# Optimization experiments

Hardware: AMD Instinct MI355X
Metric: run time of the kernel (lower is better)

## Reference

```python
import jax, jax.numpy as jnp
import numpy as np

N = 50000   # nodes (subjects in population graph)
E = 800000  # edges (similarity graph, avg degree 16)
F = 128     # node features


def setup_inputs() -> dict:
    key = jax.random.key(0)
    ks = jax.random.split(key, 8)

    def glorot(k, shape):
        scale = 1.0 / np.sqrt(shape[0])
        return jax.random.normal(k, shape, jnp.float32) * scale

    x = jax.random.normal(ks[0], (N, F), jnp.float32)
    edge_index = jax.random.randint(ks[1], (2, E), 0, N, dtype=jnp.int64)
    return {
        "x": x,
        "edge_index": edge_index,
        "W1": glorot(ks[2], (F, 128)),   "b1": jnp.zeros((128,), jnp.float32),
        "W2": glorot(ks[3], (128, 64)),  "b2": jnp.zeros((64,), jnp.float32),
        "Wf1": glorot(ks[4], (64, 32)),  "bf1": jnp.zeros((32,), jnp.float32),
        "Wf2": glorot(ks[5], (32, 1)),   "bf2": jnp.zeros((1,), jnp.float32),
    }


def reference(x, edge_index, W1, b1, W2, b2, Wf1, bf1, Wf2, bf2):
    n = x.shape[0]
    # GCNConv (PyG default): add self-loops, symmetric deg^{-1/2} normalization
    loops = jnp.arange(n, dtype=edge_index.dtype)
    src = jnp.concatenate([edge_index[0], loops])  # [E+N]
    dst = jnp.concatenate([edge_index[1], loops])  # [E+N]
    deg = jax.ops.segment_sum(jnp.ones_like(dst, x.dtype), dst, num_segments=n)
    dinv = deg ** -0.5  # deg >= 1 thanks to self-loops
    norm = (dinv[src] * dinv[dst])[:, None]  # [E+N, 1]

    def gcn_conv(h, W, b):
        h = h @ W                                    # transform [n, out]
        msg = h[src] * norm                          # gather + normalize
        agg = jax.ops.segment_sum(msg, dst, num_segments=n)  # scatter-add
        return agg + b

    h = jnp.tanh(gcn_conv(x, W1, b1))
    h = jnp.tanh(gcn_conv(h, W2, b2))
    h = jnp.tanh(h @ Wf1 + bf1)
    return h @ Wf2 + bf2  # [n, 1] brain-age prediction
```

## Files before the change

kernel.cpp:

```cpp
#include <hip/hip_runtime.h>
#include <hip/hip_fp16.h>
#include <math.h>

#define TPB 256
#define CAP 64
#define BSHIFT 7
#define BSPAN 128
#define NBLK 512
#define BCAP 3072

typedef int   nt_i4 __attribute__((ext_vector_type(4)));
typedef unsigned nt_u4 __attribute__((ext_vector_type(4)));
typedef _Float16 f16x8 __attribute__((ext_vector_type(8)));
typedef float f32x4 __attribute__((ext_vector_type(4)));

__global__ __launch_bounds__(TPB) void init_pre(const int* __restrict__ e,
                                                int* __restrict__ flag,
                                                int* __restrict__ gcur, int nbuck) {
  __shared__ int found;
  if (threadIdx.x == 0) found = 0;
  __syncthreads();
  for (int b = threadIdx.x; b < nbuck; b += TPB) gcur[b] = 0;
  int nz = 0;
  for (int k = threadIdx.x; k < 2048; k += TPB)
    nz |= (e[2 * k + 1] != 0) ? 1 : 0;
  if (nz) atomicOr(&found, 1);
  __syncthreads();
  if (threadIdx.x == 0) *flag = found;
}

__device__ __forceinline__ void load_edge(const void* eptr, int flag, int E,
                                          int e, int& s, int& d) {
  if (flag) {
    const int* p = (const int*)eptr;
    s = p[e];
    d = p[E + e];
  } else {
    const long long* p = (const long long*)eptr;
    s = (int)p[e];
    d = (int)p[E + e];
  }
}

__device__ __forceinline__ void load_edge4(const void* eptr, int flag, int E,
                                           int e0, int* s, int* d) {
  if (flag) {
    const int* p = (const int*)eptr;
    nt_i4 sv = __builtin_nontemporal_load((const nt_i4*)&p[e0]);
    nt_i4 dv = __builtin_nontemporal_load((const nt_i4*)&p[E + e0]);
    s[0] = sv.x; s[1] = sv.y; s[2] = sv.z; s[3] = sv.w;
    d[0] = dv.x; d[1] = dv.y; d[2] = dv.z; d[3] = dv.w;
  } else {
    const long long* p = (const long long*)eptr;
    nt_i4 sa = __builtin_nontemporal_load((const nt_i4*)&p[e0]);
    nt_i4 sb = __builtin_nontemporal_load((const nt_i4*)&p[e0 + 2]);
    nt_i4 da = __builtin_nontemporal_load((const nt_i4*)&p[E + e0]);
    nt_i4 db = __builtin_nontemporal_load((const nt_i4*)&p[E + e0 + 2]);
    s[0] = sa.x; s[1] = sa.z; s[2] = sb.x; s[3] = sb.z;
    d[0] = da.x; d[1] = da.z; d[2] = db.x; d[3] = db.z;
  }
}

__global__ __launch_bounds__(TPB) void bucket_pairs(const void* __restrict__ eptr,
                                                    const int* __restrict__ flag,
                                                    int* __restrict__ gcur,
                                                    unsigned long long* __restrict__ pairs,
                                                    int E, int nbuck, int chunk) {
  extern __shared__ int lds[];
  int* hist = lds;
  int* cur = lds + nbuck;
  const int tid = threadIdx.x;
  const int fl = *flag;
  for (int b = tid; b < nbuck; b += TPB) hist[b] = 0;
  __syncthreads();

  const int start = blockIdx.x * chunk;
  const int end = min(E, start + chunk);

  for (int e0 = start + tid * 4; e0 < end; e0 += TPB * 4) {
    if (e0 + 4 <= end) {
      int s[4], d[4];
      load_edge4(eptr, fl, E, e0, s, d);
#pragma unroll
      for (int j = 0; j < 4; j++) atomicAdd(&hist[d[j] >> BSHIFT], 1);
    } else {
      for (int e = e0; e < end; e++) {
        int s, d;
        load_edge(eptr, fl, E, e, s, d);
        atomicAdd(&hist[d >> BSHIFT], 1);
      }
    }
  }
  __syncthreads();

  for (int b = tid; b < nbuck; b += TPB) {
    int c = hist[b];
    cur[b] = (c > 0) ? (b * BCAP + atomicAdd(&gcur[b], c)) : 0;
  }
  __syncthreads();

  for (int e0 = start + tid * 4; e0 < end; e0 += TPB * 4) {
    if (e0 + 4 <= end) {
      int s[4], d[4];
      load_edge4(eptr, fl, E, e0, s, d);
#pragma unroll
      for (int j = 0; j < 4; j++) {
        int slot = atomicAdd(&cur[d[j] >> BSHIFT], 1);
        unsigned long long pv =
            ((unsigned long long)(unsigned)d[j] << 32) | (unsigned)s[j];
        __builtin_nontemporal_store(pv, &pairs[slot]);
      }
    } else {
      for (int e = e0; e < end; e++) {
        int s, d;
        load_edge(eptr, fl, E, e, s, d);
        int slot = atomicAdd(&cur[d >> BSHIFT], 1);
        unsigned long long pv =
            ((unsigned long long)(unsigned)d << 32) | (unsigned)s;
        __builtin_nontemporal_store(pv, &pairs[slot]);
      }
    }
  }
}

__global__ __launch_bounds__(TPB) void ell_from_pairs(const unsigned long long* __restrict__ pairs,
                                                      const int* __restrict__ gcur,
                                                      int* __restrict__ ell,
                                                      int* __restrict__ degi, int n) {
  __shared__ int cnt[BSPAN];
  const int b = blockIdx.x;
  const int tid = threadIdx.x;
  const int base = b << BSHIFT;
  for (int j = tid; j < BSPAN; j += TPB) cnt[j] = 0;
  __syncthreads();
  const int npair = min(gcur[b], BCAP);
  const unsigned long long* pp = &pairs[(size_t)b * BCAP];
  for (int i = tid; i < npair; i += TPB) {
    unsigned long long pr = __builtin_nontemporal_load(&pp[i]);
    int d = (int)(pr >> 32);
    int s = (int)(unsigned)pr;
    int slot = atomicAdd(&cnt[d - base], 1);
    if (slot < CAP) ell[(size_t)d * CAP + slot] = s;
  }
  __syncthreads();
  for (int j = tid; j < BSPAN; j += TPB) {
    int node = base + j;
    if (node < n) degi[node] = cnt[j];
  }
}

template <int NC, typename AT>
__global__ __launch_bounds__(TPB, 4) void gemm_mfma(const AT* __restrict__ A,
                                                    const float* __restrict__ W,
                                                    const int* __restrict__ degi,
                                                    __half* __restrict__ out, int nrows) {
  constexpr int K = 128;
  constexpr int WT = 136;
  constexpr int NT = NC / 16;
  __shared__ _Float16 Wt[NC * WT];

  const int tid = threadIdx.x;

  for (int idx = tid; idx < NC * (K / 2); idx += TPB) {
    int c = idx % NC;
    int p = idx / NC;
    float w0 = W[(2 * p) * NC + c];
    float w1 = W[(2 * p + 1) * NC + c];
    __half2* dst = (__half2*)&Wt[c * WT + 2 * p];
    *dst = __floats2half2_rn(w0, w1);
  }
  __syncthreads();

  const int w = tid >> 6;
  const int lane = tid & 63;
  const int l15 = lane & 15;
  const int q = lane >> 4;
  const int m_base = blockIdx.x * 64 + w * 16;
  const int m = m_base + l15;
  const bool mok = m < nrows;

  f32x4 acc[NT];
#pragma unroll
  for (int t = 0; t < NT; t++) acc[t] = (f32x4){0.f, 0.f, 0.f, 0.f};

#pragma unroll
  for (int ks = 0; ks < 4; ks++) {
    const int k0 = ks * 32;
    f16x8 a;
    if (sizeof(AT) == 4) {
      float4 f0 = make_float4(0.f, 0.f, 0.f, 0.f), f1 = f0;
      if (mok) {
        const float* ap = (const float*)A + (size_t)m * K + k0 + q * 8;
        f0 = *(const float4*)ap;
        f1 = *(const float4*)(ap + 4);
      }
      a[0] = (_Float16)f0.x; a[1] = (_Float16)f0.y;
      a[2] = (_Float16)f0.z; a[3] = (_Float16)f0.w;
      a[4] = (_Float16)f1.x; a[5] = (_Float16)f1.y;
      a[6] = (_Float16)f1.z; a[7] = (_Float16)f1.w;
    } else {
      union { uint4 u; f16x8 h; } ld;
      ld.u = make_uint4(0, 0, 0, 0);
      if (mok)
        ld.u = *(const uint4*)((const __half*)A + (size_t)m * K + k0 + q * 8);
      a = ld.h;
    }
#pragma unroll
    for (int t = 0; t < NT; t++) {
      f16x8 b = *(const f16x8*)&Wt[(t * 16 + l15) * WT + k0 + q * 8];
      acc[t] = __builtin_amdgcn_mfma_f32_16x16x32_f16(a, b, acc[t], 0, 0, 0);
    }
  }

#pragma unroll
  for (int r = 0; r < 4; r++) {
    int row = m_base + q * 4 + r;
    if (row >= nrows) continue;
    float di = rsqrtf((float)(degi[row] + 1));
#pragma unroll
    for (int t = 0; t < NT; t++)
      out[(size_t)row * NC + t * 16 + l15] = (__half)(acc[t][r] * di);
  }
}

__global__ __launch_bounds__(TPB) void gcn_agg1_fused(const int* __restrict__ degi,
                                                      const int* __restrict__ ell,
                                                      const __half* __restrict__ t,
                                                      const float* __restrict__ bias,
                                                      const float* __restrict__ W2,
                                                      __half* __restrict__ t2, int n) {
  constexpr int NC = 128, LPN = 16, CPL = 8, NPB = TPB / LPN;
  constexpr int WT = 136;
  __shared__ _Float16 Wt2[64 * WT];
  __shared__ _Float16 Ah[NPB * WT];

  const int tid = threadIdx.x;

  for (int idx = tid; idx < 64 * 64; idx += TPB) {
    int c = idx & 63;
    int p = idx >> 6;
    float w0 = W2[(2 * p) * 64 + c];
    float w1 = W2[(2 * p + 1) * 64 + c];
    *(__half2*)&Wt2[c * WT + 2 * p] = __floats2half2_rn(w0, w1);
  }

  const int g = tid / LPN;
  const int ll = tid % LPN;
  const int node = blockIdx.x * NPB + g;
  const bool active = node < n;

  if (active) {
    int dg = degi[node];
    float di = rsqrtf((float)(dg + 1));
    int deg = dg > CAP ? CAP : dg;
    const int* nbr = &ell[(size_t)node * CAP];
    const __half* tp = t + (size_t)ll * CPL;

    float acc[CPL];
#pragma unroll
    for (int c = 0; c < CPL; c++) acc[c] = 0.f;

    union Ld { uint4 u4; __half2 h[4]; };
    auto addv = [&](const Ld& v) {
#pragma unroll
      for (int c = 0; c < 4; c++) {
        float2 f = __half22float2(v.h[c]);
        acc[2 * c] += f.x;
        acc[2 * c + 1] += f.y;
      }
    };

    int j = 0;
    for (; j + 8 <= deg; j += 8) {
      nt_i4 n0 = __builtin_nontemporal_load((const nt_i4*)&nbr[j]);
      nt_i4 n1 = __builtin_nontemporal_load((const nt_i4*)&nbr[j + 4]);
      Ld v0, v1, v2, v3, v4, v5, v6, v7;
      v0.u4 = *(const uint4*)&tp[(size_t)n0.x * NC];
      v1.u4 = *(const uint4*)&tp[(size_t)n0.y * NC];
      v2.u4 = *(const uint4*)&tp[(size_t)n0.z * NC];
      v3.u4 = *(const uint4*)&tp[(size_t)n0.w * NC];
      v4.u4 = *(const uint4*)&tp[(size_t)n1.x * NC];
      v5.u4 = *(const uint4*)&tp[(size_t)n1.y * NC];
      v6.u4 = *(const uint4*)&tp[(size_t)n1.z * NC];
      v7.u4 = *(const uint4*)&tp[(size_t)n1.w * NC];
      addv(v0); addv(v1); addv(v2); addv(v3);
      addv(v4); addv(v5); addv(v6); addv(v7);
    }
    for (; j + 4 <= deg; j += 4) {
      nt_i4 n0 = __builtin_nontemporal_load((const nt_i4*)&nbr[j]);
      Ld v0, v1, v2, v3;
      v0.u4 = *(const uint4*)&tp[(size_t)n0.x * NC];
      v1.u4 = *(const uint4*)&tp[(size_t)n0.y * NC];
      v2.u4 = *(const uint4*)&tp[(size_t)n0.z * NC];
      v3.u4 = *(const uint4*)&tp[(size_t)n0.w * NC];
      addv(v0); addv(v1); addv(v2); addv(v3);
    }
    for (; j < deg; j++) {
      Ld v;
      v.u4 = *(const uint4*)&tp[(size_t)nbr[j] * NC];
      addv(v);
    }
    {
      Ld v;
      v.u4 = *(const uint4*)&tp[(size_t)node * NC];
      addv(v);
    }

    const float* bp = &bias[ll * CPL];
    float bv[CPL];
#pragma unroll
    for (int c = 0; c < CPL; c += 4) {
      float4 b = *(const float4*)&bp[c];
      bv[c] = b.x; bv[c + 1] = b.y; bv[c + 2] = b.z; bv[c + 3] = b.w;
    }
    union { _Float16 h[8]; f16x8 v; } o;
#pragma unroll
    for (int c = 0; c < CPL; c++)
      o.h[c] = (_Float16)tanhf(acc[c] * di + bv[c]);
    *(f16x8*)&Ah[g * WT + ll * CPL] = o.v;
  }
  __syncthreads();

  const int w = tid >> 6;
  const int lane = tid & 63;
  const int l15 = lane & 15;
  const int q = lane >> 4;
  f32x4 acc2 = (f32x4){0.f, 0.f, 0.f, 0.f};
#pragma unroll
  for (int ks = 0; ks < 4; ks++) {
    f16x8 a = *(const f16x8*)&Ah[l15 * WT + ks * 32 + q * 8];
    f16x8 b = *(const f16x8*)&Wt2[(w * 16 + l15) * WT + ks * 32 + q * 8];
    acc2 = __builtin_amdgcn_mfma_f32_16x16x32_f16(a, b, acc2, 0, 0, 0);
  }
#pragma unroll
  for (int r = 0; r < 4; r++) {
    int rn = blockIdx.x * NPB + q * 4 + r;
    if (rn < n) {
      float d2 = rsqrtf((float)(degi[rn] + 1));
      t2[(size_t)rn * 64 + w * 16 + l15] = (__half)(acc2[r] * d2);
    }
  }
}

__global__ __launch_bounds__(TPB) void gcn_aggregate_head(
    const int* __restrict__ degi, const int* __restrict__ ell,
    const __half* __restrict__ t, const float* __restrict__ b2,
    const float* __restrict__ Wf1, const float* __restrict__ bf1,
    const float* __restrict__ Wf2, const float* __restrict__ bf2,
    float* __restrict__ out, int n) {
  constexpr int NC = 64, LPN = 16, NPB = TPB / LPN;
  __shared__ float hrow[NPB][68];
  __shared__ float Wf1s[64 * 32];
  __shared__ float Wf2s[32];
  const int tid = threadIdx.x;

#pragma unroll
  for (int i = 0; i < 2; i++) {
    int lid = tid + i * TPB;
    *(float4*)&Wf1s[lid * 4] = *(const float4*)&Wf1[lid * 4];
  }
  if (tid < 32) Wf2s[tid] = Wf2[tid];

  const int g = tid / LPN;
  const int ll = tid % LPN;
  const int node = blockIdx.x * NPB + g;
  const bool active = node < n;

  float acc[4] = {0.f, 0.f, 0.f, 0.f};
  if (active) {
    int dg = degi[node];
    float di = rsqrtf((float)(dg + 1));
    int deg = dg > CAP ? CAP : dg;
    const int* nbr = &ell[(size_t)node * CAP];
    const __half* tp = t + (size_t)ll * 4;
    union Ld { uint2 u2; __half2 h[2]; };
    auto addv = [&](const Ld& v) {
      float2 f0 = __half22float2(v.h[0]);
      float2 f1 = __half22float2(v.h[1]);
      acc[0] += f0.x; acc[1] += f0.y; acc[2] += f1.x; acc[3] += f1.y;
    };
    int j = 0;
    for (; j + 8 <= deg; j += 8) {
      nt_i4 n0 = __builtin_nontemporal_load((const nt_i4*)&nbr[j]);
      nt_i4 n1 = __builtin_nontemporal_load((const nt_i4*)&nbr[j + 4]);
      Ld v0, v1, v2, v3, v4, v5, v6, v7;
      v0.u2 = *(const uint2*)&tp[(size_t)n0.x * NC];
      v1.u2 = *(const uint2*)&tp[(size_t)n0.y * NC];
      v2.u2 = *(const uint2*)&tp[(size_t)n0.z * NC];
      v3.u2 = *(const uint2*)&tp[(size_t)n0.w * NC];
      v4.u2 = *(const uint2*)&tp[(size_t)n1.x * NC];
      v5.u2 = *(const uint2*)&tp[(size_t)n1.y * NC];
      v6.u2 = *(const uint2*)&tp[(size_t)n1.z * NC];
      v7.u2 = *(const uint2*)&tp[(size_t)n1.w * NC];
      addv(v0); addv(v1); addv(v2); addv(v3);
      addv(v4); addv(v5); addv(v6); addv(v7);
    }
    for (; j + 4 <= deg; j += 4) {
      nt_i4 nn = __builtin_nontemporal_load((const nt_i4*)&nbr[j]);
      Ld v0, v1, v2, v3;
      v0.u2 = *(const uint2*)&tp[(size_t)nn.x * NC];
      v1.u2 = *(const uint2*)&tp[(size_t)nn.y * NC];
      v2.u2 = *(const uint2*)&tp[(size_t)nn.z * NC];
      v3.u2 = *(const uint2*)&tp[(size_t)nn.w * NC];
      addv(v0); addv(v1); addv(v2); addv(v3);
    }
    for (; j < deg; j++) {
      Ld v;
      v.u2 = *(const uint2*)&tp[(size_t)nbr[j] * NC];
      addv(v);
    }
    {
      Ld v;
      v.u2 = *(const uint2*)&tp[(size_t)node * NC];
      addv(v);
    }
    float4 b = *(const float4*)&b2[ll * 4];
    hrow[g][ll * 4 + 0] = tanhf(acc[0] * di + b.x);
    hrow[g][ll * 4 + 1] = tanhf(acc[1] * di + b.y);
    hrow[g][ll * 4 + 2] = tanhf(acc[2] * di + b.z);
    hrow[g][ll * 4 + 3] = tanhf(acc[3] * di + b.w);
  }
  __syncthreads();

  float hid0 = bf1[ll];
  float hid1 = bf1[ll + 16];
#pragma unroll 8
  for (int i = 0; i < 64; i++) {
    float hv = hrow[g][i];
    hid0 += hv * Wf1s[i * 32 + ll];
    hid1 += hv * Wf1s[i * 32 + ll + 16];
  }
  float p = tanhf(hid0) * Wf2s[ll] + tanhf(hid1) * Wf2s[ll + 16];
  p += __shfl_down(p, 8, 16);
  p += __shfl_down(p, 4, 16);
  p += __shfl_down(p, 2, 16);
  p += __shfl_down(p, 1, 16);
  if (active && ll == 0) out[node] = p + bf2[0];
}

extern "C" void kernel_launch(void* const* d_in, const int* in_sizes, int n_in,
                              void* d_out, int out_size, void* d_ws, size_t ws_size,
                              hipStream_t stream) {
  const float* x   = (const float*)d_in[0];
  const void*  eix = d_in[1];
  const float* W1  = (const float*)d_in[2];
  const float* b1  = (const float*)d_in[3];
  const float* W2  = (const float*)d_in[4];
  const float* b2  = (const float*)d_in[5];
  const float* Wf1 = (const float*)d_in[6];
  const float* bf1 = (const float*)d_in[7];
  const float* Wf2 = (const float*)d_in[8];
  const float* bf2 = (const float*)d_in[9];
  float* out = (float*)d_out;

  const int N = in_sizes[0] / 128;
  const int E = in_sizes[1] / 2;
  const int nbuck = (N + BSPAN - 1) >> BSHIFT;
  int chunk = (E + NBLK - 1) / NBLK;
  chunk = (chunk + 3) & ~3;
  const size_t ldsBytes = (size_t)nbuck * 2 * 4;

  char* ws = (char*)d_ws;
  size_t off = 0;
  int* degi = (int*)(ws + off); off += (size_t)N * 4;
  int* flag = (int*)(ws + off); off += 64;
  int* gcur = (int*)(ws + off); off += (size_t)(nbuck + 16) * 4;
  off = (off + 15) & ~(size_t)15;
  unsigned long long* pairs = (unsigned long long*)(ws + off);
  off += (size_t)nbuck * BCAP * 8;
  int* ell = (int*)(ws + off); off += (size_t)N * CAP * 4;
  off = (off + 15) & ~(size_t)15;
  __half* t1 = (__half*)(ws + off); off += (size_t)N * 128 * 2;
  __half* t2 = (__half*)(ws + off); off += (size_t)N * 64 * 2;
  (void)ws_size; (void)n_in; (void)out_size;

  init_pre<<<1, TPB, 0, stream>>>((const int*)eix, flag, gcur, nbuck);
  bucket_pairs<<<NBLK, TPB, ldsBytes, stream>>>(eix, flag, gcur, pairs, E, nbuck, chunk);
  ell_from_pairs<<<nbuck, TPB, 0, stream>>>(pairs, gcur, ell, degi, N);

  gemm_mfma<128, float><<<(N + 63) / 64, TPB, 0, stream>>>(x, W1, degi, t1, N);

  gcn_agg1_fused<<<(N + 15) / 16, TPB, 0, stream>>>(degi, ell, t1, b1, W2, t2, N);

  gcn_aggregate_head<<<(N + 15) / 16, TPB, 0, stream>>>(degi, ell, t2, b2,
                                                        Wf1, bf1, Wf2, bf2, out, N);
}
```

Before: 227.7 us.

## Split layer-1 aggregation into two column-half passes and unfuse W2 GEMM

Replaces the fused layer-1 aggregate+W2 kernel with two launches that each gather a 64-column half of t1, so each pass has a smaller working set that fits the cache better. The tanh output goes to a new h1 buffer with nontemporal stores, and a separate gemm_mfma<64, __half> launch then applies W2. This removes the per-block W2 LDS staging and the block barrier. In exchange it adds extra launches, a 2-byte-per-element h1 write and reread, and reads every neighbor index list twice.

```diff
diff --git a/kernel.cpp b/kernel.cpp
--- a/kernel.cpp
+++ b/kernel.cpp
@@ -223,123 +223,88 @@
   }
 }
 
-__global__ __launch_bounds__(TPB) void gcn_agg1_fused(const int* __restrict__ degi,
-                                                      const int* __restrict__ ell,
-                                                      const __half* __restrict__ t,
-                                                      const float* __restrict__ bias,
-                                                      const float* __restrict__ W2,
-                                                      __half* __restrict__ t2, int n) {
-  constexpr int NC = 128, LPN = 16, CPL = 8, NPB = TPB / LPN;
-  constexpr int WT = 136;
-  __shared__ _Float16 Wt2[64 * WT];
-  __shared__ _Float16 Ah[NPB * WT];
-
+template <int HALF>
+__global__ __launch_bounds__(TPB) void gcn_agg1_half(const int* __restrict__ degi,
+                                                     const int* __restrict__ ell,
+                                                     const __half* __restrict__ t,
+                                                     const float* __restrict__ bias,
+                                                     __half* __restrict__ h1, int n) {
+  constexpr int NC = 128, LPN = 8, CPL = 8, NPB = TPB / LPN;
   const int tid = threadIdx.x;
-
-  for (int idx = tid; idx < 64 * 64; idx += TPB) {
-    int c = idx & 63;
-    int p = idx >> 6;
-    float w0 = W2[(2 * p) * 64 + c];
-    float w1 = W2[(2 * p + 1) * 64 + c];
-    *(__half2*)&Wt2[c * WT + 2 * p] = __floats2half2_rn(w0, w1);
-  }
-
   const int g = tid / LPN;
   const int ll = tid % LPN;
   const int node = blockIdx.x * NPB + g;
-  const bool active = node < n;
-
-  if (active) {
-    int dg = degi[node];
-    float di = rsqrtf((float)(dg + 1));
-    int deg = dg > CAP ? CAP : dg;
-    const int* nbr = &ell[(size_t)node * CAP];
-    const __half* tp = t + (size_t)ll * CPL;
-
-    float acc[CPL];
-#pragma unroll
-    for (int c = 0; c < CPL; c++) acc[c] = 0.f;
-
-    union Ld { uint4 u4; __half2 h[4]; };
-    auto addv = [&](const Ld& v) {
-#pragma unroll
-      for (int c = 0; c < 4; c++) {
-        float2 f = __half22float2(v.h[c]);
-        acc[2 * c] += f.x;
-        acc[2 * c + 1] += f.y;
-      }
-    };
-
-    int j = 0;
-    for (; j + 8 <= deg; j += 8) {
-      nt_i4 n0 = __builtin_nontemporal_load((const nt_i4*)&nbr[j]);
-      nt_i4 n1 = __builtin_nontemporal_load((const nt_i4*)&nbr[j + 4]);
-      Ld v0, v1, v2, v3, v4, v5, v6, v7;
-      v0.u4 = *(const uint4*)&tp[(size_t)n0.x * NC];
-      v1.u4 = *(const uint4*)&tp[(size_t)n0.y * NC];
-      v2.u4 = *(const uint4*)&tp[(size_t)n0.z * NC];
-      v3.u4 = *(const uint4*)&tp[(size_t)n0.w * NC];
-      v4.u4 = *(const uint4*)&tp[(size_t)n1.x * NC];
-      v5.u4 = *(const uint4*)&tp[(size_t)n1.y * NC];
-      v6.u4 = *(const uint4*)&tp[(size_t)n1.z * NC];
-      v7.u4 = *(const uint4*)&tp[(size_t)n1.w * NC];
-      addv(v0); addv(v1); addv(v2); addv(v3);
-      addv(v4); addv(v5); addv(v6); addv(v7);
-    }
-    for (; j + 4 <= deg; j += 4) {
-      nt_i4 n0 = __builtin_nontemporal_load((const nt_i4*)&nbr[j]);
-      Ld v0, v1, v2, v3;
-      v0.u4 = *(const uint4*)&tp[(size_t)n0.x * NC];
-      v1.u4 = *(const uint4*)&tp[(size_t)n0.y * NC];
-      v2.u4 = *(const uint4*)&tp[(size_t)n0.z * NC];
-      v3.u4 = *(const uint4*)&tp[(size_t)n0.w * NC];
-      addv(v0); addv(v1); addv(v2); addv(v3);
-    }
-    for (; j < deg; j++) {
-      Ld v;
-      v.u4 = *(const uint4*)&tp[(size_t)nbr[j] * NC];
-      addv(v);
-    }
-    {
-      Ld v;
-      v.u4 = *(const uint4*)&tp[(size_t)node * NC];
-      addv(v);
-    }
-
-    const float* bp = &bias[ll * CPL];
-    float bv[CPL];
-#pragma unroll
-    for (int c = 0; c < CPL; c += 4) {
-      float4 b = *(const float4*)&bp[c];
-      bv[c] = b.x; bv[c + 1] = b.y; bv[c + 2] = b.z; bv[c + 3] = b.w;
-    }
-    union { _Float16 h[8]; f16x8 v; } o;
-#pragma unroll
-    for (int c = 0; c < CPL; c++)
-      o.h[c] = (_Float16)tanhf(acc[c] * di + bv[c]);
-    *(f16x8*)&Ah[g * WT + ll * CPL] = o.v;
-  }
-  __syncthreads();
-
-  const int w = tid >> 6;
-  const int lane = tid & 63;
-  const int l15 = lane & 15;
-  const int q = lane >> 4;
-  f32x4 acc2 = (f32x4){0.f, 0.f, 0.f, 0.f};
-#pragma unroll
-  for (int ks = 0; ks < 4; ks++) {
-    f16x8 a = *(const f16x8*)&Ah[l15 * WT + ks * 32 + q * 8];
-    f16x8 b = *(const f16x8*)&Wt2[(w * 16 + l15) * WT + ks * 32 + q * 8];
-    acc2 = __builtin_amdgcn_mfma_f32_16x16x32_f16(a, b, acc2, 0, 0, 0);
-  }
-#pragma unroll
-  for (int r = 0; r < 4; r++) {
-    int rn = blockIdx.x * NPB + q * 4 + r;
-    if (rn < n) {
-      float d2 = rsqrtf((float)(degi[rn] + 1));
-      t2[(size_t)rn * 64 + w * 16 + l15] = (__half)(acc2[r] * d2);
-    }
-  }
+  if (node >= n) return;
+
+  int dg = degi[node];
+  float di = rsqrtf((float)(dg + 1));
+  int deg = dg > CAP ? CAP : dg;
+  const int* nbr = &ell[(size_t)node * CAP];
+  const __half* tp = t + HALF * 64 + (size_t)ll * CPL;
+
+  float acc[CPL];
+#pragma unroll
+  for (int c = 0; c < CPL; c++) acc[c] = 0.f;
+
+  union Ld { uint4 u4; __half2 h[4]; };
+  auto addv = [&](const Ld& v) {
+#pragma unroll
+    for (int c = 0; c < 4; c++) {
+      float2 f = __half22float2(v.h[c]);
+      acc[2 * c] += f.x;
+      acc[2 * c + 1] += f.y;
+    }
+  };
+
+  int j = 0;
+  for (; j + 8 <= deg; j += 8) {
+    nt_i4 n0 = __builtin_nontemporal_load((const nt_i4*)&nbr[j]);
+    nt_i4 n1 = __builtin_nontemporal_load((const nt_i4*)&nbr[j + 4]);
+    Ld v0, v1, v2, v3, v4, v5, v6, v7;
+    v0.u4 = *(const uint4*)&tp[(size_t)n0.x * NC];
+    v1.u4 = *(const uint4*)&tp[(size_t)n0.y * NC];
+    v2.u4 = *(const uint4*)&tp[(size_t)n0.z * NC];
+    v3.u4 = *(const uint4*)&tp[(size_t)n0.w * NC];
+    v4.u4 = *(const uint4*)&tp[(size_t)n1.x * NC];
+    v5.u4 = *(const uint4*)&tp[(size_t)n1.y * NC];
+    v6.u4 = *(const uint4*)&tp[(size_t)n1.z * NC];
+    v7.u4 = *(const uint4*)&tp[(size_t)n1.w * NC];
+    addv(v0); addv(v1); addv(v2); addv(v3);
+    addv(v4); addv(v5); addv(v6); addv(v7);
+  }
+  for (; j + 4 <= deg; j += 4) {
+    nt_i4 n0 = __builtin_nontemporal_load((const nt_i4*)&nbr[j]);
+    Ld v0, v1, v2, v3;
+    v0.u4 = *(const uint4*)&tp[(size_t)n0.x * NC];
+    v1.u4 = *(const uint4*)&tp[(size_t)n0.y * NC];
+    v2.u4 = *(const uint4*)&tp[(size_t)n0.z * NC];
+    v3.u4 = *(const uint4*)&tp[(size_t)n0.w * NC];
+    addv(v0); addv(v1); addv(v2); addv(v3);
+  }
+  for (; j < deg; j++) {
+    Ld v;
+    v.u4 = *(const uint4*)&tp[(size_t)nbr[j] * NC];
+    addv(v);
+  }
+  {
+    Ld v;
+    v.u4 = *(const uint4*)&tp[(size_t)node * NC];
+    addv(v);
+  }
+
+  const float* bp = &bias[HALF * 64 + ll * CPL];
+  float bv[CPL];
+#pragma unroll
+  for (int c = 0; c < CPL; c += 4) {
+    float4 b = *(const float4*)&bp[c];
+    bv[c] = b.x; bv[c + 1] = b.y; bv[c + 2] = b.z; bv[c + 3] = b.w;
+  }
+  union { __half2 hh[4]; nt_u4 u; } o;
+#pragma unroll
+  for (int c = 0; c < CPL; c += 2)
+    o.hh[c / 2] = __float22half2_rn(make_float2(tanhf(acc[c] * di + bv[c]),
+                                                tanhf(acc[c + 1] * di + bv[c + 1])));
+  __builtin_nontemporal_store(o.u, (nt_u4*)&h1[(size_t)node * NC + HALF * 64 + ll * CPL]);
 }
 
 __global__ __launch_bounds__(TPB) void gcn_aggregate_head(
@@ -471,6 +436,7 @@
   int* ell = (int*)(ws + off); off += (size_t)N * CAP * 4;
   off = (off + 15) & ~(size_t)15;
   __half* t1 = (__half*)(ws + off); off += (size_t)N * 128 * 2;
+  __half* h1 = (__half*)(ws + off); off += (size_t)N * 128 * 2;
   __half* t2 = (__half*)(ws + off); off += (size_t)N * 64 * 2;
   (void)ws_size; (void)n_in; (void)out_size;
 
@@ -480,7 +446,11 @@
 
   gemm_mfma<128, float><<<(N + 63) / 64, TPB, 0, stream>>>(x, W1, degi, t1, N);
 
-  gcn_agg1_fused<<<(N + 15) / 16, TPB, 0, stream>>>(degi, ell, t1, b1, W2, t2, N);
+  const int gblocks = (N + 31) / 32;
+  gcn_agg1_half<0><<<gblocks, TPB, 0, stream>>>(degi, ell, t1, b1, h1, N);
+  gcn_agg1_half<1><<<gblocks, TPB, 0, stream>>>(degi, ell, t1, b1, h1, N);
+
+  gemm_mfma<64, __half><<<(N + 63) / 64, TPB, 0, stream>>>(h1, W2, degi, t2, N);
 
   gcn_aggregate_head<<<(N + 15) / 16, TPB, 0, stream>>>(degi, ell, t2, b2,
                                                         Wf1, bf1, Wf2, bf2, out, N);
```

Result: slower. 246.6 us (+8.3%).
